# Performance work log

Measured on AMD Instinct MI355X. Metric: run time of the kernel, lower is better.

The kernel has to match this reference:

```python
import jax, jax.numpy as jnp
import numpy as np

N = 20000
E = 320000
IN_C = 256
HID = 64
OUT_C = 64
NUM_LAYERS = 3
HEADS = 8


def setup_inputs() -> dict:
    key = jax.random.key(0)
    ks = jax.random.split(key, 12)
    s_in = 1.0 / np.sqrt(IN_C)
    s_h = 1.0 / np.sqrt(HID)
    inp = {
        "x": jax.random.normal(ks[0], (N, IN_C), dtype=jnp.float32),
        "edge_index": jax.random.randint(ks[1], (2, E), 0, N, dtype=jnp.int64),
        "lin1_w": jax.random.uniform(ks[2], (IN_C, HID), jnp.float32, -s_in, s_in),
        "lin1_b": jnp.zeros((HID,), jnp.float32),
        "wq": jax.random.uniform(ks[3], (NUM_LAYERS, HID, HID), jnp.float32, -s_h, s_h),
        "bq": jnp.zeros((NUM_LAYERS, HID), jnp.float32),
        "wk": jax.random.uniform(ks[4], (NUM_LAYERS, HID, HID), jnp.float32, -s_h, s_h),
        "bk": jnp.zeros((NUM_LAYERS, HID), jnp.float32),
        "wv": jax.random.uniform(ks[5], (NUM_LAYERS, HID, HID), jnp.float32, -s_h, s_h),
        "bv": jnp.zeros((NUM_LAYERS, HID), jnp.float32),
        "lin2_w": jax.random.uniform(ks[6], (HID, OUT_C), jnp.float32, -s_h, s_h),
        "lin2_b": jnp.zeros((OUT_C,), jnp.float32),
    }
    return inp


def reference(x, edge_index, lin1_w, lin1_b, wq, bq, wk, bk, wv, bv, lin2_w, lin2_b):
    n = x.shape[0]
    C = lin1_w.shape[1]
    d = C // HEADS  # per-head dim
    inv_sqrt_d = 1.0 / (d ** 0.5)

    # gcn_norm with self-loops (symmetric normalization, edge weights = 1)
    loop = jnp.arange(n, dtype=edge_index.dtype)
    row = jnp.concatenate([edge_index[0], loop])  # source j
    col = jnp.concatenate([edge_index[1], loop])  # target i
    deg = jax.ops.segment_sum(jnp.ones_like(col, dtype=x.dtype), col, num_segments=n)
    dinv = jnp.where(deg > 0, deg ** -0.5, 0.0)
    norm = dinv[row] * dinv[col]  # [E+N]

    # input projection (dropout inactive in eval mode)
    h = jax.nn.relu(x @ lin1_w + lin1_b)
    x_all = h[:, None, :]  # [N, 1, C] growing history

    for l in range(NUM_LAYERS):
        t = x_all.shape[1]
        # node-level projections (linear commutes with gather)
        q = x_all[:, -1] @ wq[l] + bq[l]                      # [N, C]
        k = jnp.einsum("ntc,cd->ntd", x_all, wk[l]) + bk[l]   # [N, t, C]
        v = jnp.einsum("ntc,cd->ntd", x_all, wv[l]) + bv[l]   # [N, t, C]
        # per-edge multi-head attention of target's latest repr over source history
        Qe = q[col].reshape(-1, HEADS, d)                      # [E', H, d]
        Ke = k[row].reshape(-1, t, HEADS, d)                   # [E', t, H, d]
        Ve = v[row].reshape(-1, t, HEADS, d)
        scores = jnp.einsum("ehd,ethd->eht", Qe, Ke) * inv_sqrt_d
        attn = jax.nn.softmax(scores, axis=-1)                 # [E', H, t]
        msg = jnp.einsum("eht,ethd->ehd", attn, Ve).reshape(-1, C)
        msg = msg * norm[:, None]
        out = jax.ops.segment_sum(msg, col, num_segments=n)    # sum aggregation
        out = jax.nn.relu(out)
        x_all = jnp.concatenate([x_all, out[:, None, :]], axis=1)

    logits = x_all[:, -1] @ lin2_w + lin2_b
    return jax.nn.log_softmax(logits, axis=1)
```

## Files before the change

### kernel.cpp

```cpp
#include <hip/hip_runtime.h>
#include <math.h>

#define HID 64
#define HEADS 8
#define NUM_LAYERS 3

typedef __attribute__((ext_vector_type(8))) short bf16x8;
typedef __attribute__((ext_vector_type(4))) float f32x4;

__device__ __forceinline__ unsigned short f2bf(float f) {
    union { float f; unsigned int u; } cv; cv.f = f;
    unsigned int u = cv.u;
    unsigned int r = (u + 0x7FFFu + ((u >> 16) & 1u)) >> 16;
    return (unsigned short)r;
}
__device__ __forceinline__ float bflo(unsigned int u) {
    union { unsigned int u; float f; } cv; cv.u = u << 16; return cv.f;
}
__device__ __forceinline__ float bfhi(unsigned int u) {
    union { unsigned int u; float f; } cv; cv.u = u & 0xFFFF0000u; return cv.f;
}
__device__ __forceinline__ unsigned relu_pk(unsigned u) {
    unsigned m = ((u & 0x8000u) ? 0u : 0xFFFFu) |
                 ((u & 0x80000000u) ? 0u : 0xFFFF0000u);
    return u & m;
}

__global__ void k_count(const int* __restrict__ col, int* __restrict__ counts, int E) {
    int e = blockIdx.x * blockDim.x + threadIdx.x;
    if (e < E) atomicAdd(&counts[col[e]], 1);
}

__global__ __launch_bounds__(1024) void k_scan(const int* __restrict__ counts,
                                               int* __restrict__ start,
                                               float* __restrict__ dinv, int n) {
    __shared__ int wsum[16];
    int tid = threadIdx.x;
    int lane = tid & 63, wv = tid >> 6;
    int ipt = (n + 1023) >> 10;
    int c0 = tid * ipt;
    int c1 = min(n, c0 + ipt);
    int s = 0;
    for (int i = c0; i < c1; ++i) s += counts[i];
    int x = s;
#pragma unroll
    for (int off = 1; off < 64; off <<= 1) {
        int y = __shfl_up(x, off);
        if (lane >= off) x += y;
    }
    if (lane == 63) wsum[wv] = x;
    __syncthreads();
    if (wv == 0 && lane < 16) {
        int t2 = wsum[lane];
#pragma unroll
        for (int off = 1; off < 16; off <<= 1) {
            int y = __shfl_up(t2, off);
            if (lane >= off) t2 += y;
        }
        wsum[lane] = t2;
    }
    __syncthreads();
    int waveoff = (wv > 0) ? wsum[wv - 1] : 0;
    int run = waveoff + x - s;
    for (int i = c0; i < c1; ++i) {
        int v = counts[i];
        start[i] = run;
        dinv[i] = rsqrtf((float)(v + 1));
        run += v;
    }
    if (tid == 0) start[n] = wsum[15];
}

__global__ void k_scatter(const int* __restrict__ ei, const int* __restrict__ start,
                          int* __restrict__ fill, int* __restrict__ ebuf, int E) {
    int e = blockIdx.x * blockDim.x + threadIdx.x;
    if (e >= E) return;
    int r = ei[e], c = ei[E + e];
    int pos = start[c] + atomicAdd(&fill[c], 1);
    ebuf[pos] = r;
}

#define ALD 72

__device__ __forceinline__ void stage_w_bf16(unsigned short* Wt,
                                             const float* __restrict__ w, int tid) {
    for (int idx = tid; idx < 1024; idx += 256) {
        int k = idx >> 4, n4 = (idx & 15) * 4;
        float4 wv = *(const float4*)&w[k * 64 + n4];
        Wt[(n4 + 0) * ALD + k] = f2bf(wv.x);
        Wt[(n4 + 1) * ALD + k] = f2bf(wv.y);
        Wt[(n4 + 2) * ALD + k] = f2bf(wv.z);
        Wt[(n4 + 3) * ALD + k] = f2bf(wv.w);
    }
}

__device__ __forceinline__ void mfma_step(const unsigned short* Alds,
                                          const unsigned short* Wt,
                                          int tid, f32x4 acc[4]) {
    int lane = tid & 63;
    int m0 = (tid >> 6) * 16;
    int c16 = lane & 15, quad = lane >> 4;
    const unsigned short* ar = &Alds[(m0 + c16) * ALD + quad * 8];
    bf16x8 a0 = *(const bf16x8*)ar;
    bf16x8 a1 = *(const bf16x8*)(ar + 32);
#pragma unroll
    for (int nt = 0; nt < 4; ++nt) {
        const unsigned short* br = &Wt[(nt * 16 + c16) * ALD + quad * 8];
        bf16x8 b0 = *(const bf16x8*)br;
        bf16x8 b1 = *(const bf16x8*)(br + 32);
        acc[nt] = __builtin_amdgcn_mfma_f32_16x16x32_bf16(a0, b0, acc[nt], 0, 0, 0);
        acc[nt] = __builtin_amdgcn_mfma_f32_16x16x32_bf16(a1, b1, acc[nt], 0, 0, 0);
    }
}

__global__ __launch_bounds__(256, 4) void k_lin1(
    const float* __restrict__ x, const float* __restrict__ w,
    const float* __restrict__ b, const float* __restrict__ wv0,
    const float* __restrict__ bv0, unsigned short* __restrict__ h,
    unsigned short* __restrict__ kv, int n) {
    __shared__ __align__(16) unsigned short Alds[64 * ALD];
    __shared__ __align__(16) unsigned short Wt[64 * ALD];
    int tid = threadIdx.x;
    int node0 = blockIdx.x * 64;
    f32x4 acc[4];
#pragma unroll
    for (int nt = 0; nt < 4; ++nt) acc[nt] = (f32x4){0.f, 0.f, 0.f, 0.f};

    for (int kc = 0; kc < 256; kc += 64) {
        __syncthreads();
        stage_w_bf16(Wt, w + kc * 64, tid);
        for (int idx = tid; idx < 1024; idx += 256) {
            int r = idx >> 4, c4 = (idx & 15) * 4;
            int node = node0 + r;
            float4 v = make_float4(0.f, 0.f, 0.f, 0.f);
            if (node < n) v = *(const float4*)&x[(size_t)node * 256 + kc + c4];
            Alds[r * ALD + c4 + 0] = f2bf(v.x);
            Alds[r * ALD + c4 + 1] = f2bf(v.y);
            Alds[r * ALD + c4 + 2] = f2bf(v.z);
            Alds[r * ALD + c4 + 3] = f2bf(v.w);
        }
        __syncthreads();
        mfma_step(Alds, Wt, tid, acc);
    }
    int lane = tid & 63;
    int m0 = (tid >> 6) * 16, c16 = lane & 15, quad = lane >> 4;
    float bias[4];
#pragma unroll
    for (int nt = 0; nt < 4; ++nt) bias[nt] = b[nt * 16 + c16];

    __syncthreads();
    stage_w_bf16(Wt, wv0, tid);
#pragma unroll
    for (int i = 0; i < 4; ++i) {
        int row = m0 + quad * 4 + i;
        int node = node0 + row;
#pragma unroll
        for (int nt = 0; nt < 4; ++nt) {
            unsigned short hb = f2bf(fmaxf(acc[nt][i] + bias[nt], 0.f));
            Alds[row * ALD + nt * 16 + c16] = hb;
            if (node < n) h[(size_t)node * 64 + nt * 16 + c16] = hb;
        }
    }
    __syncthreads();
    f32x4 acc2[4];
#pragma unroll
    for (int nt = 0; nt < 4; ++nt) acc2[nt] = (f32x4){0.f, 0.f, 0.f, 0.f};
    mfma_step(Alds, Wt, tid, acc2);
    float bias2[4];
#pragma unroll
    for (int nt = 0; nt < 4; ++nt) bias2[nt] = bv0[nt * 16 + c16];
#pragma unroll
    for (int i = 0; i < 4; ++i) {
        int node = node0 + m0 + quad * 4 + i;
        if (node < n) {
#pragma unroll
            for (int nt = 0; nt < 4; ++nt)
                kv[(size_t)node * 64 + nt * 16 + c16] = f2bf(acc2[nt][i] + bias2[nt]);
        }
    }
}

__global__ __launch_bounds__(256, 4) void k_qkv(
    const unsigned short* __restrict__ xsbase,
    const float* __restrict__ wq, const float* __restrict__ bq,
    const float* __restrict__ wk, const float* __restrict__ bk,
    const float* __restrict__ wv, const float* __restrict__ bv,
    float* __restrict__ q, unsigned short* __restrict__ kv,
    int n, int layer, int t, int kv_stride) {
    int job = blockIdx.y;
    const unsigned short* src; const float* w; const float* b; bool relu_in;
    int kv_off = 0;
    if (job == 0) {
        src = xsbase + (size_t)layer * n * 64;
        w = wq + layer * 4096; b = bq + layer * 64;
        relu_in = (layer >= 1);
    } else if (job <= t) {
        int s = job - 1;
        src = xsbase + (size_t)s * n * 64;
        w = wk + layer * 4096; b = bk + layer * 64;
        kv_off = s * 128;
        relu_in = (s >= 1);
    } else {
        int s = job - t - 1;
        src = xsbase + (size_t)s * n * 64;
        w = wv + layer * 4096; b = bv + layer * 64;
        kv_off = s * 128 + 64;
        relu_in = (s >= 1);
    }
    __shared__ __align__(16) unsigned short Alds[64 * ALD];
    __shared__ __align__(16) unsigned short Wt[64 * ALD];
    int tid = threadIdx.x;
    int node0 = blockIdx.x * 64;
    stage_w_bf16(Wt, w, tid);
    for (int idx = tid; idx < 512; idx += 256) {
        int r = idx >> 3, seg = idx & 7;
        int node = node0 + r;
        uint4 u = make_uint4(0u, 0u, 0u, 0u);
        if (node < n) u = *(const uint4*)&src[(size_t)node * 64 + seg * 8];
        if (relu_in) {
            u.x = relu_pk(u.x); u.y = relu_pk(u.y);
            u.z = relu_pk(u.z); u.w = relu_pk(u.w);
        }
        *(uint4*)&Alds[r * ALD + seg * 8] = u;
    }
    __syncthreads();
    f32x4 acc[4];
#pragma unroll
    for (int nt = 0; nt < 4; ++nt) acc[nt] = (f32x4){0.f, 0.f, 0.f, 0.f};
    mfma_step(Alds, Wt, tid, acc);

    int lane = tid & 63;
    int m0 = (tid >> 6) * 16, c16 = lane & 15, quad = lane >> 4;
    float bias[4];
#pragma unroll
    for (int nt = 0; nt < 4; ++nt) bias[nt] = b[nt * 16 + c16];
    if (job == 0) {
#pragma unroll
        for (int i = 0; i < 4; ++i) {
            int node = node0 + m0 + quad * 4 + i;
            if (node < n) {
#pragma unroll
                for (int nt = 0; nt < 4; ++nt)
                    q[(size_t)node * 64 + nt * 16 + c16] = acc[nt][i] + bias[nt];
            }
        }
    } else {
#pragma unroll
        for (int i = 0; i < 4; ++i) {
            int node = node0 + m0 + quad * 4 + i;
            if (node < n) {
#pragma unroll
                for (int nt = 0; nt < 4; ++nt)
                    kv[(size_t)node * kv_stride + kv_off + nt * 16 + c16] =
                        f2bf(acc[nt][i] + bias[nt]);
            }
        }
    }
}

template <int T>
__global__ __launch_bounds__(256) void k_attn_g(
    const int* __restrict__ start, const int* __restrict__ ebuf,
    const float* __restrict__ dinv, const float* __restrict__ q,
    const unsigned short* __restrict__ kv, unsigned short* __restrict__ outp, int n) {
    const int KVS = (T == 1) ? 64 : T * 128;
    int node = (int)((blockIdx.x * (size_t)blockDim.x + threadIdx.x) >> 6);
    int lane = threadIdx.x & 63;
    if (node >= n) return;
    int g = lane >> 3;
    int cb = (lane & 7) * 8;
    const float isd = 0.35355339059327373f;

    float qv[8];
    if (T > 1) {
        float4 q0 = *(const float4*)&q[(size_t)node * 64 + cb];
        float4 q1 = *(const float4*)&q[(size_t)node * 64 + cb + 4];
        qv[0] = q0.x; qv[1] = q0.y; qv[2] = q0.z; qv[3] = q0.w;
        qv[4] = q1.x; qv[5] = q1.y; qv[6] = q1.z; qv[7] = q1.w;
    }
    float dc = dinv[node];
    int s0 = start[node];
    int cnt = start[node + 1] - s0 + 1;

    float acc[8];
#pragma unroll
    for (int k = 0; k < 8; ++k) acc[k] = 0.f;

    for (int base = 0; base < cnt; base += 8) {
        int idx = base + g;
        bool valid = idx < cnt;
        int r = node;
        if (valid && idx > 0) r = ebuf[s0 + idx - 1];
        float dr = valid ? dinv[r] : 0.f;
        const unsigned short* rkv = kv + (size_t)r * KVS;

        float sc[T];
        float wgt;
        if (T > 1) {
            float m = -1e30f;
#pragma unroll
            for (int s = 0; s < T; ++s) {
                uint4 ku = *(const uint4*)&rkv[s * 128 + cb];
                float p = qv[0] * bflo(ku.x) + qv[1] * bfhi(ku.x)
                        + qv[2] * bflo(ku.y) + qv[3] * bfhi(ku.y)
                        + qv[4] * bflo(ku.z) + qv[5] * bfhi(ku.z)
                        + qv[6] * bflo(ku.w) + qv[7] * bfhi(ku.w);
                p *= isd;
                sc[s] = p;
                m = fmaxf(m, p);
            }
            float denom = 0.f;
#pragma unroll
            for (int s = 0; s < T; ++s) { sc[s] = __expf(sc[s] - m); denom += sc[s]; }
            wgt = dr / denom;
        } else {
            sc[0] = 1.f;
            wgt = dr;
        }

        float mg[8];
#pragma unroll
        for (int k = 0; k < 8; ++k) mg[k] = 0.f;
#pragma unroll
        for (int s = 0; s < T; ++s) {
            uint4 vu = *(const uint4*)&rkv[((T == 1) ? 0 : s * 128 + 64) + cb];
            float wv_ = sc[s];
            mg[0] += wv_ * bflo(vu.x); mg[1] += wv_ * bfhi(vu.x);
            mg[2] += wv_ * bflo(vu.y); mg[3] += wv_ * bfhi(vu.y);
            mg[4] += wv_ * bflo(vu.z); mg[5] += wv_ * bfhi(vu.z);
            mg[6] += wv_ * bflo(vu.w); mg[7] += wv_ * bfhi(vu.w);
        }
#pragma unroll
        for (int k = 0; k < 8; ++k) acc[k] += wgt * mg[k];
    }

#pragma unroll
    for (int off = 8; off < 64; off <<= 1) {
#pragma unroll
        for (int k = 0; k < 8; ++k) acc[k] += __shfl_xor(acc[k], off);
    }
    if (g == 0) {
        ushort4 o0, o1;
        o0.x = f2bf(acc[0] * dc); o0.y = f2bf(acc[1] * dc);
        o0.z = f2bf(acc[2] * dc); o0.w = f2bf(acc[3] * dc);
        o1.x = f2bf(acc[4] * dc); o1.y = f2bf(acc[5] * dc);
        o1.z = f2bf(acc[6] * dc); o1.w = f2bf(acc[7] * dc);
        *(ushort4*)&outp[(size_t)node * 64 + cb] = o0;
        *(ushort4*)&outp[(size_t)node * 64 + cb + 4] = o1;
    }
}

__global__ __launch_bounds__(256) void k_attn3f(
    const int* __restrict__ start, const int* __restrict__ ebuf,
    const float* __restrict__ dinv, const float* __restrict__ q,
    const unsigned short* __restrict__ kv,
    const float* __restrict__ w2, const float* __restrict__ b2,
    float* __restrict__ outp, int n) {
    const int T = 3, KVS = 384;
    int node = (int)((blockIdx.x * (size_t)blockDim.x + threadIdx.x) >> 6);
    int lane = threadIdx.x & 63;
    if (node >= n) return;
    int g = lane >> 3;
    int cb = (lane & 7) * 8;
    const float isd = 0.35355339059327373f;

    float qv[8];
    {
        float4 q0 = *(const float4*)&q[(size_t)node * 64 + cb];
        float4 q1 = *(const float4*)&q[(size_t)node * 64 + cb + 4];
        qv[0] = q0.x; qv[1] = q0.y; qv[2] = q0.z; qv[3] = q0.w;
        qv[4] = q1.x; qv[5] = q1.y; qv[6] = q1.z; qv[7] = q1.w;
    }
    float dc = dinv[node];
    int s0 = start[node];
    int cnt = start[node + 1] - s0 + 1;

    float acc[8];
#pragma unroll
    for (int k = 0; k < 8; ++k) acc[k] = 0.f;

    for (int base = 0; base < cnt; base += 8) {
        int idx = base + g;
        bool valid = idx < cnt;
        int r = node;
        if (valid && idx > 0) r = ebuf[s0 + idx - 1];
        float dr = valid ? dinv[r] : 0.f;
        const unsigned short* rkv = kv + (size_t)r * KVS;

        float sc[T];
        float m = -1e30f;
#pragma unroll
        for (int s = 0; s < T; ++s) {
            uint4 ku = *(const uint4*)&rkv[s * 128 + cb];
            float p = qv[0] * bflo(ku.x) + qv[1] * bfhi(ku.x)
                    + qv[2] * bflo(ku.y) + qv[3] * bfhi(ku.y)
                    + qv[4] * bflo(ku.z) + qv[5] * bfhi(ku.z)
                    + qv[6] * bflo(ku.w) + qv[7] * bfhi(ku.w);
            p *= isd;
            sc[s] = p;
            m = fmaxf(m, p);
        }
        float denom = 0.f;
#pragma unroll
        for (int s = 0; s < T; ++s) { sc[s] = __expf(sc[s] - m); denom += sc[s]; }
        float wgt = dr / denom;

        float mg[8];
#pragma unroll
        for (int k = 0; k < 8; ++k) mg[k] = 0.f;
#pragma unroll
        for (int s = 0; s < T; ++s) {
            uint4 vu = *(const uint4*)&rkv[s * 128 + 64 + cb];
            float wv_ = sc[s];
            mg[0] += wv_ * bflo(vu.x); mg[1] += wv_ * bfhi(vu.x);
            mg[2] += wv_ * bflo(vu.y); mg[3] += wv_ * bfhi(vu.y);
            mg[4] += wv_ * bflo(vu.z); mg[5] += wv_ * bfhi(vu.z);
            mg[6] += wv_ * bflo(vu.w); mg[7] += wv_ * bfhi(vu.w);
        }
#pragma unroll
        for (int k = 0; k < 8; ++k) acc[k] += wgt * mg[k];
    }

#pragma unroll
    for (int off = 8; off < 64; off <<= 1) {
#pragma unroll
        for (int k = 0; k < 8; ++k) acc[k] += __shfl_xor(acc[k], off);
    }
    float lg = b2[lane];
#pragma unroll
    for (int c = 0; c < 64; ++c) {
        float xc = fmaxf(__shfl(acc[c & 7], c >> 3) * dc, 0.f);
        lg += xc * w2[c * 64 + lane];
    }
    float mx = lg;
#pragma unroll
    for (int off = 1; off < 64; off <<= 1) mx = fmaxf(mx, __shfl_xor(mx, off));
    float e = __expf(lg - mx);
    float ssum = e;
#pragma unroll
    for (int off = 1; off < 64; off <<= 1) ssum += __shfl_xor(ssum, off);
    outp[(size_t)node * 64 + lane] = lg - mx - __logf(ssum);
}

extern "C" void kernel_launch(void* const* d_in, const int* in_sizes, int n_in,
                              void* d_out, int out_size, void* d_ws, size_t ws_size,
                              hipStream_t stream) {
    const float* x  = (const float*)d_in[0];
    const int*   ei = (const int*)d_in[1];
    const float* w1 = (const float*)d_in[2];
    const float* b1 = (const float*)d_in[3];
    const float* wq = (const float*)d_in[4];
    const float* bq = (const float*)d_in[5];
    const float* wk = (const float*)d_in[6];
    const float* bk = (const float*)d_in[7];
    const float* wv = (const float*)d_in[8];
    const float* bv = (const float*)d_in[9];
    const float* w2 = (const float*)d_in[10];
    const float* b2 = (const float*)d_in[11];
    float* outp = (float*)d_out;

    int n = in_sizes[0] / 256;
    int E = in_sizes[1] / 2;

    float* ws = (float*)d_ws;
    size_t off = 0;
    float* dinv = ws + off; off += (size_t)n;
    float* q    = ws + off; off += (size_t)n * 64;
    unsigned short* xsU = (unsigned short*)(ws + off); off += (size_t)n * 96;
    unsigned short* kvU = (unsigned short*)(ws + off); off += (size_t)n * 192;
    int* wsI    = (int*)(ws + off);
    int* counts = wsI;
    int* fill   = wsI + n;
    int* startA = wsI + 2 * n;
    int* ebuf   = wsI + 3 * n + 1;

    hipMemsetAsync(counts, 0, 2 * (size_t)n * sizeof(int), stream);
    k_count<<<(E + 255) / 256, 256, 0, stream>>>(ei + E, counts, E);
    k_scan<<<1, 1024, 0, stream>>>(counts, startA, dinv, n);
    k_scatter<<<(E + 255) / 256, 256, 0, stream>>>(ei, startA, fill, ebuf, E);

    k_lin1<<<(n + 63) / 64, 256, 0, stream>>>(x, w1, b1, wv, bv, xsU, kvU, n);

    int attn_grid = (int)(((size_t)n * 64 + 255) / 256);

    k_attn_g<1><<<attn_grid, 256, 0, stream>>>(startA, ebuf, dinv, q, kvU,
                                               xsU + (size_t)n * 64, n);
    {
        dim3 grid((n + 63) / 64, 5);
        k_qkv<<<grid, 256, 0, stream>>>(xsU, wq, bq, wk, bk, wv, bv,
                                        q, kvU, n, 1, 2, 256);
        k_attn_g<2><<<attn_grid, 256, 0, stream>>>(startA, ebuf, dinv, q, kvU,
                                                   xsU + (size_t)n * 128, n);
    }
    {
        dim3 grid((n + 63) / 64, 7);
        k_qkv<<<grid, 256, 0, stream>>>(xsU, wq, bq, wk, bk, wv, bv,
                                        q, kvU, n, 2, 3, 384);
        k_attn3f<<<attn_grid, 256, 0, stream>>>(startA, ebuf, dinv, q, kvU,
                                                w2, b2, outp, n);
    }
}
```

Before: 265.6 us.

## Fold K/V projections into per-node query and aggregate raw history features

Removes the separate QKV projection kernels and K/V buffers. Each target node computes its own q, pre-multiplies it by Wk to get q', and scores each edge directly against the source's raw bf16 history (the bk term is dropped since it is constant across t and cancels in softmax). The attention-weighted history is aggregated, and Wv plus bias is applied once per node after summation. This trades per-node recompute and 64-step shuffle matvecs for much less gathered memory per edge. Edges are now processed serially per wave instead of 8 at a time, with shuffle reductions per edge, which lengthens the loop.

```diff
diff --git a/kernel.cpp b/kernel.cpp
--- a/kernel.cpp
+++ b/kernel.cpp
@@ -3,7 +3,7 @@
 
 #define HID 64
 #define HEADS 8
-#define NUM_LAYERS 3
+#define ALD 72
 
 typedef __attribute__((ext_vector_type(8))) short bf16x8;
 typedef __attribute__((ext_vector_type(4))) float f32x4;
@@ -20,10 +20,17 @@
 __device__ __forceinline__ float bfhi(unsigned int u) {
     union { unsigned int u; float f; } cv; cv.u = u & 0xFFFF0000u; return cv.f;
 }
-__device__ __forceinline__ unsigned relu_pk(unsigned u) {
-    unsigned m = ((u & 0x8000u) ? 0u : 0xFFFFu) |
-                 ((u & 0x80000000u) ? 0u : 0xFFFF0000u);
-    return u & m;
+
+__device__ __forceinline__ float dot8(const float* qp, uint4 u) {
+    return qp[0] * bflo(u.x) + qp[1] * bfhi(u.x) + qp[2] * bflo(u.y) +
+           qp[3] * bfhi(u.y) + qp[4] * bflo(u.z) + qp[5] * bfhi(u.z) +
+           qp[6] * bflo(u.w) + qp[7] * bfhi(u.w);
+}
+__device__ __forceinline__ void axpy8(float a, uint4 u, float* Y) {
+    Y[0] += a * bflo(u.x); Y[1] += a * bfhi(u.x);
+    Y[2] += a * bflo(u.y); Y[3] += a * bfhi(u.y);
+    Y[4] += a * bflo(u.z); Y[5] += a * bfhi(u.z);
+    Y[6] += a * bflo(u.w); Y[7] += a * bfhi(u.w);
 }
 
 __global__ void k_count(const int* __restrict__ col, int* __restrict__ counts, int E) {
@@ -36,7 +43,7 @@
                                                float* __restrict__ dinv, int n) {
     __shared__ int wsum[16];
     int tid = threadIdx.x;
-    int lane = tid & 63, wv = tid >> 6;
+    int lane = tid & 63, wvi = tid >> 6;
     int ipt = (n + 1023) >> 10;
     int c0 = tid * ipt;
     int c1 = min(n, c0 + ipt);
@@ -48,9 +55,9 @@
         int y = __shfl_up(x, off);
         if (lane >= off) x += y;
     }
-    if (lane == 63) wsum[wv] = x;
+    if (lane == 63) wsum[wvi] = x;
     __syncthreads();
-    if (wv == 0 && lane < 16) {
+    if (wvi == 0 && lane < 16) {
         int t2 = wsum[lane];
 #pragma unroll
         for (int off = 1; off < 16; off <<= 1) {
@@ -60,7 +67,7 @@
         wsum[lane] = t2;
     }
     __syncthreads();
-    int waveoff = (wv > 0) ? wsum[wv - 1] : 0;
+    int waveoff = (wvi > 0) ? wsum[wvi - 1] : 0;
     int run = waveoff + x - s;
     for (int i = c0; i < c1; ++i) {
         int v = counts[i];
@@ -79,8 +86,6 @@
     int pos = start[c] + atomicAdd(&fill[c], 1);
     ebuf[pos] = r;
 }
-
-#define ALD 72
 
 __device__ __forceinline__ void stage_w_bf16(unsigned short* Wt,
                                              const float* __restrict__ w, int tid) {
@@ -115,9 +120,7 @@
 
 __global__ __launch_bounds__(256, 4) void k_lin1(
     const float* __restrict__ x, const float* __restrict__ w,
-    const float* __restrict__ b, const float* __restrict__ wv0,
-    const float* __restrict__ bv0, unsigned short* __restrict__ h,
-    unsigned short* __restrict__ kv, int n) {
+    const float* __restrict__ b, unsigned short* __restrict__ h, int n) {
     __shared__ __align__(16) unsigned short Alds[64 * ALD];
     __shared__ __align__(16) unsigned short Wt[64 * ALD];
     int tid = threadIdx.x;
@@ -147,299 +150,134 @@
     float bias[4];
 #pragma unroll
     for (int nt = 0; nt < 4; ++nt) bias[nt] = b[nt * 16 + c16];
-
-    __syncthreads();
-    stage_w_bf16(Wt, wv0, tid);
-#pragma unroll
-    for (int i = 0; i < 4; ++i) {
-        int row = m0 + quad * 4 + i;
-        int node = node0 + row;
-#pragma unroll
-        for (int nt = 0; nt < 4; ++nt) {
-            unsigned short hb = f2bf(fmaxf(acc[nt][i] + bias[nt], 0.f));
-            Alds[row * ALD + nt * 16 + c16] = hb;
-            if (node < n) h[(size_t)node * 64 + nt * 16 + c16] = hb;
-        }
-    }
-    __syncthreads();
-    f32x4 acc2[4];
-#pragma unroll
-    for (int nt = 0; nt < 4; ++nt) acc2[nt] = (f32x4){0.f, 0.f, 0.f, 0.f};
-    mfma_step(Alds, Wt, tid, acc2);
-    float bias2[4];
-#pragma unroll
-    for (int nt = 0; nt < 4; ++nt) bias2[nt] = bv0[nt * 16 + c16];
 #pragma unroll
     for (int i = 0; i < 4; ++i) {
         int node = node0 + m0 + quad * 4 + i;
         if (node < n) {
 #pragma unroll
             for (int nt = 0; nt < 4; ++nt)
-                kv[(size_t)node * 64 + nt * 16 + c16] = f2bf(acc2[nt][i] + bias2[nt]);
-        }
-    }
-}
-
-__global__ __launch_bounds__(256, 4) void k_qkv(
-    const unsigned short* __restrict__ xsbase,
+                h[(size_t)node * 64 + nt * 16 + c16] =
+                    f2bf(fmaxf(acc[nt][i] + bias[nt], 0.f));
+        }
+    }
+}
+
+template <int T, bool FINAL>
+__device__ __forceinline__ void attn_x_body(
+    int node, int lane, const int* __restrict__ start,
+    const int* __restrict__ ebuf, const float* __restrict__ dinv,
+    unsigned short* __restrict__ xs, size_t sstride,
     const float* __restrict__ wq, const float* __restrict__ bq,
-    const float* __restrict__ wk, const float* __restrict__ bk,
-    const float* __restrict__ wv, const float* __restrict__ bv,
-    float* __restrict__ q, unsigned short* __restrict__ kv,
-    int n, int layer, int t, int kv_stride) {
-    int job = blockIdx.y;
-    const unsigned short* src; const float* w; const float* b; bool relu_in;
-    int kv_off = 0;
-    if (job == 0) {
-        src = xsbase + (size_t)layer * n * 64;
-        w = wq + layer * 4096; b = bq + layer * 64;
-        relu_in = (layer >= 1);
-    } else if (job <= t) {
-        int s = job - 1;
-        src = xsbase + (size_t)s * n * 64;
-        w = wk + layer * 4096; b = bk + layer * 64;
-        kv_off = s * 128;
-        relu_in = (s >= 1);
-    } else {
-        int s = job - t - 1;
-        src = xsbase + (size_t)s * n * 64;
-        w = wv + layer * 4096; b = bv + layer * 64;
-        kv_off = s * 128 + 64;
-        relu_in = (s >= 1);
-    }
-    __shared__ __align__(16) unsigned short Alds[64 * ALD];
-    __shared__ __align__(16) unsigned short Wt[64 * ALD];
-    int tid = threadIdx.x;
-    int node0 = blockIdx.x * 64;
-    stage_w_bf16(Wt, w, tid);
-    for (int idx = tid; idx < 512; idx += 256) {
-        int r = idx >> 3, seg = idx & 7;
-        int node = node0 + r;
-        uint4 u = make_uint4(0u, 0u, 0u, 0u);
-        if (node < n) u = *(const uint4*)&src[(size_t)node * 64 + seg * 8];
-        if (relu_in) {
-            u.x = relu_pk(u.x); u.y = relu_pk(u.y);
-            u.z = relu_pk(u.z); u.w = relu_pk(u.w);
-        }
-        *(uint4*)&Alds[r * ALD + seg * 8] = u;
-    }
-    __syncthreads();
-    f32x4 acc[4];
-#pragma unroll
-    for (int nt = 0; nt < 4; ++nt) acc[nt] = (f32x4){0.f, 0.f, 0.f, 0.f};
-    mfma_step(Alds, Wt, tid, acc);
-
-    int lane = tid & 63;
-    int m0 = (tid >> 6) * 16, c16 = lane & 15, quad = lane >> 4;
-    float bias[4];
-#pragma unroll
-    for (int nt = 0; nt < 4; ++nt) bias[nt] = b[nt * 16 + c16];
-    if (job == 0) {
-#pragma unroll
-        for (int i = 0; i < 4; ++i) {
-            int node = node0 + m0 + quad * 4 + i;
-            if (node < n) {
-#pragma unroll
-                for (int nt = 0; nt < 4; ++nt)
-                    q[(size_t)node * 64 + nt * 16 + c16] = acc[nt][i] + bias[nt];
-            }
-        }
-    } else {
-#pragma unroll
-        for (int i = 0; i < 4; ++i) {
-            int node = node0 + m0 + quad * 4 + i;
-            if (node < n) {
-#pragma unroll
-                for (int nt = 0; nt < 4; ++nt)
-                    kv[(size_t)node * kv_stride + kv_off + nt * 16 + c16] =
-                        f2bf(acc[nt][i] + bias[nt]);
-            }
-        }
-    }
-}
-
-template <int T>
-__global__ __launch_bounds__(256) void k_attn_g(
-    const int* __restrict__ start, const int* __restrict__ ebuf,
-    const float* __restrict__ dinv, const float* __restrict__ q,
-    const unsigned short* __restrict__ kv, unsigned short* __restrict__ outp, int n) {
-    const int KVS = (T == 1) ? 64 : T * 128;
-    int node = (int)((blockIdx.x * (size_t)blockDim.x + threadIdx.x) >> 6);
-    int lane = threadIdx.x & 63;
-    if (node >= n) return;
-    int g = lane >> 3;
-    int cb = (lane & 7) * 8;
-    const float isd = 0.35355339059327373f;
-
-    float qv[8];
+    const float* __restrict__ wk, const float* __restrict__ wv,
+    const float* __restrict__ bv, const float* __restrict__ w2,
+    const float* __restrict__ b2, float* __restrict__ outf) {
+    const int h8 = lane & 56;
+    const int cb = (lane & 7) * 8;
+
+    float qp[8];
     if (T > 1) {
-        float4 q0 = *(const float4*)&q[(size_t)node * 64 + cb];
-        float4 q1 = *(const float4*)&q[(size_t)node * 64 + cb + 4];
-        qv[0] = q0.x; qv[1] = q0.y; qv[2] = q0.z; qv[3] = q0.w;
-        qv[4] = q1.x; qv[5] = q1.y; qv[6] = q1.z; qv[7] = q1.w;
-    }
+        const float isd = 0.35355339059327373f;
+        uint4 xu = *(const uint4*)&xs[(size_t)(T - 1) * sstride +
+                                      (size_t)node * 64 + cb];
+        float xq[8] = {bflo(xu.x), bfhi(xu.x), bflo(xu.y), bfhi(xu.y),
+                       bflo(xu.z), bfhi(xu.z), bflo(xu.w), bfhi(xu.w)};
+        float qo = bq[lane];
+#pragma unroll
+        for (int c = 0; c < 64; ++c)
+            qo += __shfl(xq[c & 7], c >> 3) * wq[c * 64 + lane];
+        float qh[8];
+#pragma unroll
+        for (int d = 0; d < 8; ++d) qh[d] = __shfl(qo, h8 + d);
+#pragma unroll
+        for (int dp = 0; dp < 8; ++dp) {
+            const float* wr = &wk[(cb + dp) * 64 + h8];
+            float s = 0.f;
+#pragma unroll
+            for (int d = 0; d < 8; ++d) s += qh[d] * wr[d];
+            qp[dp] = s * isd;
+        }
+    }
+
     float dc = dinv[node];
     int s0 = start[node];
     int cnt = start[node + 1] - s0 + 1;
 
-    float acc[8];
-#pragma unroll
-    for (int k = 0; k < 8; ++k) acc[k] = 0.f;
-
-    for (int base = 0; base < cnt; base += 8) {
-        int idx = base + g;
-        bool valid = idx < cnt;
+    float Y[8];
+#pragma unroll
+    for (int d = 0; d < 8; ++d) Y[d] = 0.f;
+    float S = 0.f;
+
+    for (int idx = 0; idx < cnt; ++idx) {
         int r = node;
-        if (valid && idx > 0) r = ebuf[s0 + idx - 1];
-        float dr = valid ? dinv[r] : 0.f;
-        const unsigned short* rkv = kv + (size_t)r * KVS;
-
-        float sc[T];
-        float wgt;
+        if (idx > 0) r = ebuf[s0 + idx - 1];
+        float dr = dinv[r];
+        uint4 xu[T];
+#pragma unroll
+        for (int t = 0; t < T; ++t)
+            xu[t] = *(const uint4*)&xs[(size_t)t * sstride + (size_t)r * 64 + cb];
+        float coef[T];
         if (T > 1) {
-            float m = -1e30f;
-#pragma unroll
-            for (int s = 0; s < T; ++s) {
-                uint4 ku = *(const uint4*)&rkv[s * 128 + cb];
-                float p = qv[0] * bflo(ku.x) + qv[1] * bfhi(ku.x)
-                        + qv[2] * bflo(ku.y) + qv[3] * bfhi(ku.y)
-                        + qv[4] * bflo(ku.z) + qv[5] * bfhi(ku.z)
-                        + qv[6] * bflo(ku.w) + qv[7] * bfhi(ku.w);
-                p *= isd;
-                sc[s] = p;
-                m = fmaxf(m, p);
+            float p[T];
+#pragma unroll
+            for (int t = 0; t < T; ++t) p[t] = dot8(qp, xu[t]);
+#pragma unroll
+            for (int off = 1; off < 8; off <<= 1) {
+#pragma unroll
+                for (int t = 0; t < T; ++t) p[t] += __shfl_xor(p[t], off);
             }
+            float m = p[0];
+#pragma unroll
+            for (int t = 1; t < T; ++t) m = fmaxf(m, p[t]);
             float denom = 0.f;
 #pragma unroll
-            for (int s = 0; s < T; ++s) { sc[s] = __expf(sc[s] - m); denom += sc[s]; }
-            wgt = dr / denom;
+            for (int t = 0; t < T; ++t) { coef[t] = __expf(p[t] - m); denom += coef[t]; }
+            float w = dr / denom;
+#pragma unroll
+            for (int t = 0; t < T; ++t) coef[t] *= w;
         } else {
-            sc[0] = 1.f;
-            wgt = dr;
-        }
-
-        float mg[8];
-#pragma unroll
-        for (int k = 0; k < 8; ++k) mg[k] = 0.f;
-#pragma unroll
-        for (int s = 0; s < T; ++s) {
-            uint4 vu = *(const uint4*)&rkv[((T == 1) ? 0 : s * 128 + 64) + cb];
-            float wv_ = sc[s];
-            mg[0] += wv_ * bflo(vu.x); mg[1] += wv_ * bfhi(vu.x);
-            mg[2] += wv_ * bflo(vu.y); mg[3] += wv_ * bfhi(vu.y);
-            mg[4] += wv_ * bflo(vu.z); mg[5] += wv_ * bfhi(vu.z);
-            mg[6] += wv_ * bflo(vu.w); mg[7] += wv_ * bfhi(vu.w);
-        }
-#pragma unroll
-        for (int k = 0; k < 8; ++k) acc[k] += wgt * mg[k];
-    }
-
-#pragma unroll
-    for (int off = 8; off < 64; off <<= 1) {
-#pragma unroll
-        for (int k = 0; k < 8; ++k) acc[k] += __shfl_xor(acc[k], off);
-    }
-    if (g == 0) {
-        ushort4 o0, o1;
-        o0.x = f2bf(acc[0] * dc); o0.y = f2bf(acc[1] * dc);
-        o0.z = f2bf(acc[2] * dc); o0.w = f2bf(acc[3] * dc);
-        o1.x = f2bf(acc[4] * dc); o1.y = f2bf(acc[5] * dc);
-        o1.z = f2bf(acc[6] * dc); o1.w = f2bf(acc[7] * dc);
-        *(ushort4*)&outp[(size_t)node * 64 + cb] = o0;
-        *(ushort4*)&outp[(size_t)node * 64 + cb + 4] = o1;
-    }
-}
-
-__global__ __launch_bounds__(256) void k_attn3f(
+            coef[0] = dr;
+        }
+#pragma unroll
+        for (int t = 0; t < T; ++t) axpy8(coef[t], xu[t], Y);
+        S += dr;
+    }
+
+    float v = bv[lane] * S;
+#pragma unroll
+    for (int c = 0; c < 64; ++c)
+        v += __shfl(Y[c & 7], h8 | (c >> 3)) * wv[c * 64 + lane];
+    float out = fmaxf(v * dc, 0.f);
+
+    if (!FINAL) {
+        xs[(size_t)T * sstride + (size_t)node * 64 + lane] = f2bf(out);
+    } else {
+        float lg = b2[lane];
+#pragma unroll
+        for (int c = 0; c < 64; ++c)
+            lg += __shfl(out, c) * w2[c * 64 + lane];
+        float mx = lg;
+#pragma unroll
+        for (int off = 1; off < 64; off <<= 1) mx = fmaxf(mx, __shfl_xor(mx, off));
+        float e = __expf(lg - mx);
+        float ssum = e;
+#pragma unroll
+        for (int off = 1; off < 64; off <<= 1) ssum += __shfl_xor(ssum, off);
+        outf[(size_t)node * 64 + lane] = lg - mx - __logf(ssum);
+    }
+}
+
+template <int T, bool FINAL>
+__global__ __launch_bounds__(256, 4) void k_attn_x(
     const int* __restrict__ start, const int* __restrict__ ebuf,
-    const float* __restrict__ dinv, const float* __restrict__ q,
-    const unsigned short* __restrict__ kv,
-    const float* __restrict__ w2, const float* __restrict__ b2,
-    float* __restrict__ outp, int n) {
-    const int T = 3, KVS = 384;
+    const float* __restrict__ dinv, unsigned short* __restrict__ xs,
+    size_t sstride, const float* __restrict__ wq, const float* __restrict__ bq,
+    const float* __restrict__ wk, const float* __restrict__ wv,
+    const float* __restrict__ bv, const float* __restrict__ w2,
+    const float* __restrict__ b2, float* __restrict__ outf, int n) {
     int node = (int)((blockIdx.x * (size_t)blockDim.x + threadIdx.x) >> 6);
-    int lane = threadIdx.x & 63;
     if (node >= n) return;
-    int g = lane >> 3;
-    int cb = (lane & 7) * 8;
-    const float isd = 0.35355339059327373f;
-
-    float qv[8];
-    {
-        float4 q0 = *(const float4*)&q[(size_t)node * 64 + cb];
-        float4 q1 = *(const float4*)&q[(size_t)node * 64 + cb + 4];
-        qv[0] = q0.x; qv[1] = q0.y; qv[2] = q0.z; qv[3] = q0.w;
-        qv[4] = q1.x; qv[5] = q1.y; qv[6] = q1.z; qv[7] = q1.w;
-    }
-    float dc = dinv[node];
-    int s0 = start[node];
-    int cnt = start[node + 1] - s0 + 1;
-
-    float acc[8];
-#pragma unroll
-    for (int k = 0; k < 8; ++k) acc[k] = 0.f;
-
-    for (int base = 0; base < cnt; base += 8) {
-        int idx = base + g;
-        bool valid = idx < cnt;
-        int r = node;
-        if (valid && idx > 0) r = ebuf[s0 + idx - 1];
-        float dr = valid ? dinv[r] : 0.f;
-        const unsigned short* rkv = kv + (size_t)r * KVS;
-
-        float sc[T];
-        float m = -1e30f;
-#pragma unroll
-        for (int s = 0; s < T; ++s) {
-            uint4 ku = *(const uint4*)&rkv[s * 128 + cb];
-            float p = qv[0] * bflo(ku.x) + qv[1] * bfhi(ku.x)
-                    + qv[2] * bflo(ku.y) + qv[3] * bfhi(ku.y)
-                    + qv[4] * bflo(ku.z) + qv[5] * bfhi(ku.z)
-                    + qv[6] * bflo(ku.w) + qv[7] * bfhi(ku.w);
-            p *= isd;
-            sc[s] = p;
-            m = fmaxf(m, p);
-        }
-        float denom = 0.f;
-#pragma unroll
-        for (int s = 0; s < T; ++s) { sc[s] = __expf(sc[s] - m); denom += sc[s]; }
-        float wgt = dr / denom;
-
-        float mg[8];
-#pragma unroll
-        for (int k = 0; k < 8; ++k) mg[k] = 0.f;
-#pragma unroll
-        for (int s = 0; s < T; ++s) {
-            uint4 vu = *(const uint4*)&rkv[s * 128 + 64 + cb];
-            float wv_ = sc[s];
-            mg[0] += wv_ * bflo(vu.x); mg[1] += wv_ * bfhi(vu.x);
-            mg[2] += wv_ * bflo(vu.y); mg[3] += wv_ * bfhi(vu.y);
-            mg[4] += wv_ * bflo(vu.z); mg[5] += wv_ * bfhi(vu.z);
-            mg[6] += wv_ * bflo(vu.w); mg[7] += wv_ * bfhi(vu.w);
-        }
-#pragma unroll
-        for (int k = 0; k < 8; ++k) acc[k] += wgt * mg[k];
-    }
-
-#pragma unroll
-    for (int off = 8; off < 64; off <<= 1) {
-#pragma unroll
-        for (int k = 0; k < 8; ++k) acc[k] += __shfl_xor(acc[k], off);
-    }
-    float lg = b2[lane];
-#pragma unroll
-    for (int c = 0; c < 64; ++c) {
-        float xc = fmaxf(__shfl(acc[c & 7], c >> 3) * dc, 0.f);
-        lg += xc * w2[c * 64 + lane];
-    }
-    float mx = lg;
-#pragma unroll
-    for (int off = 1; off < 64; off <<= 1) mx = fmaxf(mx, __shfl_xor(mx, off));
-    float e = __expf(lg - mx);
-    float ssum = e;
-#pragma unroll
-    for (int off = 1; off < 64; off <<= 1) ssum += __shfl_xor(ssum, off);
-    outp[(size_t)node * 64 + lane] = lg - mx - __logf(ssum);
+    attn_x_body<T, FINAL>(node, threadIdx.x & 63, start, ebuf, dinv, xs, sstride,
+                          wq, bq, wk, wv, bv, w2, b2, outf);
 }
 
 extern "C" void kernel_launch(void* const* d_in, const int* in_sizes, int n_in,
@@ -458,6 +296,7 @@
     const float* w2 = (const float*)d_in[10];
     const float* b2 = (const float*)d_in[11];
     float* outp = (float*)d_out;
+    (void)bk;
 
     int n = in_sizes[0] / 256;
     int E = in_sizes[1] / 2;
@@ -465,38 +304,33 @@
     float* ws = (float*)d_ws;
     size_t off = 0;
     float* dinv = ws + off; off += (size_t)n;
-    float* q    = ws + off; off += (size_t)n * 64;
     unsigned short* xsU = (unsigned short*)(ws + off); off += (size_t)n * 96;
-    unsigned short* kvU = (unsigned short*)(ws + off); off += (size_t)n * 192;
     int* wsI    = (int*)(ws + off);
     int* counts = wsI;
     int* fill   = wsI + n;
     int* startA = wsI + 2 * n;
     int* ebuf   = wsI + 3 * n + 1;
 
+    size_t sstride = (size_t)n * 64;
+
     hipMemsetAsync(counts, 0, 2 * (size_t)n * sizeof(int), stream);
     k_count<<<(E + 255) / 256, 256, 0, stream>>>(ei + E, counts, E);
     k_scan<<<1, 1024, 0, stream>>>(counts, startA, dinv, n);
     k_scatter<<<(E + 255) / 256, 256, 0, stream>>>(ei, startA, fill, ebuf, E);
 
-    k_lin1<<<(n + 63) / 64, 256, 0, stream>>>(x, w1, b1, wv, bv, xsU, kvU, n);
+    k_lin1<<<(n + 63) / 64, 256, 0, stream>>>(x, w1, b1, xsU, n);
 
     int attn_grid = (int)(((size_t)n * 64 + 255) / 256);
 
-    k_attn_g<1><<<attn_grid, 256, 0, stream>>>(startA, ebuf, dinv, q, kvU,
-                                               xsU + (size_t)n * 64, n);
-    {
-        dim3 grid((n + 63) / 64, 5);
-        k_qkv<<<grid, 256, 0, stream>>>(xsU, wq, bq, wk, bk, wv, bv,
-                                        q, kvU, n, 1, 2, 256);
-        k_attn_g<2><<<attn_grid, 256, 0, stream>>>(startA, ebuf, dinv, q, kvU,
-                                                   xsU + (size_t)n * 128, n);
-    }
-    {
-        dim3 grid((n + 63) / 64, 7);
-        k_qkv<<<grid, 256, 0, stream>>>(xsU, wq, bq, wk, bk, wv, bv,
-                                        q, kvU, n, 2, 3, 384);
-        k_attn3f<<<attn_grid, 256, 0, stream>>>(startA, ebuf, dinv, q, kvU,
-                                                w2, b2, outp, n);
-    }
-}
+    k_attn_x<1, false><<<attn_grid, 256, 0, stream>>>(
+        startA, ebuf, dinv, xsU, sstride, nullptr, nullptr, nullptr,
+        wv, bv, nullptr, nullptr, nullptr, n);
+
+    k_attn_x<2, false><<<attn_grid, 256, 0, stream>>>(
+        startA, ebuf, dinv, xsU, sstride, wq + 4096, bq + 64, wk + 4096,
+        wv + 4096, bv + 64, nullptr, nullptr, nullptr, n);
+
+    k_attn_x<3, true><<<attn_grid, 256, 0, stream>>>(
+        startA, ebuf, dinv, xsU, sstride, wq + 8192, bq + 128, wk + 8192,
+        wv + 8192, bv + 128, w2, b2, outp, n);
+}
```

Measured after the change: 499.7 us. 1.88x slower.

## Fuse Q projection into attention, batch K/V staging, compact edge buffer

Applied to the files above, without the earlier changes.

The Q projection now runs inside the attention kernel as a per-node wave GEMV, which removes the fp32 q buffer and its round trip. The K/V projections for layers 1 and 2 that depend only on earlier states are computed together in one staged launch, so the per-layer launch only handles the newest state. The edge-source buffer is stored as 16-bit indices, the fill counter is replaced by decrementing counts, and the neighbor index load is prefetched one chunk ahead. The trade-offs are redundant Q matmul work per wave, more shuffles, and a 16-bit index that only holds for n ≤ 65536.

```diff
diff --git a/kernel.cpp b/kernel.cpp
--- a/kernel.cpp
+++ b/kernel.cpp
@@ -3,7 +3,7 @@
 
 #define HID 64
 #define HEADS 8
-#define NUM_LAYERS 3
+#define ALD 72
 
 typedef __attribute__((ext_vector_type(8))) short bf16x8;
 typedef __attribute__((ext_vector_type(4))) float f32x4;
@@ -36,7 +36,7 @@
                                                float* __restrict__ dinv, int n) {
     __shared__ int wsum[16];
     int tid = threadIdx.x;
-    int lane = tid & 63, wv = tid >> 6;
+    int lane = tid & 63, wvi = tid >> 6;
     int ipt = (n + 1023) >> 10;
     int c0 = tid * ipt;
     int c1 = min(n, c0 + ipt);
@@ -48,9 +48,9 @@
         int y = __shfl_up(x, off);
         if (lane >= off) x += y;
     }
-    if (lane == 63) wsum[wv] = x;
+    if (lane == 63) wsum[wvi] = x;
     __syncthreads();
-    if (wv == 0 && lane < 16) {
+    if (wvi == 0 && lane < 16) {
         int t2 = wsum[lane];
 #pragma unroll
         for (int off = 1; off < 16; off <<= 1) {
@@ -60,7 +60,7 @@
         wsum[lane] = t2;
     }
     __syncthreads();
-    int waveoff = (wv > 0) ? wsum[wv - 1] : 0;
+    int waveoff = (wvi > 0) ? wsum[wvi - 1] : 0;
     int run = waveoff + x - s;
     for (int i = c0; i < c1; ++i) {
         int v = counts[i];
@@ -72,15 +72,14 @@
 }
 
 __global__ void k_scatter(const int* __restrict__ ei, const int* __restrict__ start,
-                          int* __restrict__ fill, int* __restrict__ ebuf, int E) {
+                          int* __restrict__ counts, unsigned short* __restrict__ ebuf,
+                          int E) {
     int e = blockIdx.x * blockDim.x + threadIdx.x;
     if (e >= E) return;
     int r = ei[e], c = ei[E + e];
-    int pos = start[c] + atomicAdd(&fill[c], 1);
-    ebuf[pos] = r;
-}
-
-#define ALD 72
+    int pos = start[c] + atomicSub(&counts[c], 1) - 1;
+    ebuf[pos] = (unsigned short)r;
+}
 
 __device__ __forceinline__ void stage_w_bf16(unsigned short* Wt,
                                              const float* __restrict__ w, int tid) {
@@ -180,33 +179,24 @@
     }
 }
 
-__global__ __launch_bounds__(256, 4) void k_qkv(
-    const unsigned short* __restrict__ xsbase,
-    const float* __restrict__ wq, const float* __restrict__ bq,
+__global__ __launch_bounds__(256, 4) void k_stage(
+    const unsigned short* __restrict__ xs, size_t sstride,
     const float* __restrict__ wk, const float* __restrict__ bk,
     const float* __restrict__ wv, const float* __restrict__ bv,
-    float* __restrict__ q, unsigned short* __restrict__ kv,
-    int n, int layer, int t, int kv_stride) {
-    int job = blockIdx.y;
-    const unsigned short* src; const float* w; const float* b; bool relu_in;
-    int kv_off = 0;
-    if (job == 0) {
-        src = xsbase + (size_t)layer * n * 64;
-        w = wq + layer * 4096; b = bq + layer * 64;
-        relu_in = (layer >= 1);
-    } else if (job <= t) {
-        int s = job - 1;
-        src = xsbase + (size_t)s * n * 64;
-        w = wk + layer * 4096; b = bk + layer * 64;
-        kv_off = s * 128;
-        relu_in = (s >= 1);
-    } else {
-        int s = job - t - 1;
-        src = xsbase + (size_t)s * n * 64;
-        w = wv + layer * 4096; b = bv + layer * 64;
-        kv_off = s * 128 + 64;
-        relu_in = (s >= 1);
-    }
+    unsigned short* __restrict__ kv1, unsigned short* __restrict__ kv2,
+    int n, int phase) {
+    int j = blockIdx.y;
+    int layer, s, isV;
+    if (phase == 0) { layer = 1 + (j >> 2); s = j & 1; isV = (j >> 1) & 1; }
+    else            { layer = 2; s = 2; isV = j; }
+    const unsigned short* src = xs + (size_t)s * sstride;
+    const float* w = (isV ? wv : wk) + layer * 4096;
+    const float* b = (isV ? bv : bk) + layer * 64;
+    unsigned short* dst = (layer == 1) ? kv1 : kv2;
+    int stride = (layer == 1) ? 256 : 384;
+    int koff = s * 128 + (isV ? 64 : 0);
+    bool relu_in = (s >= 1);
+
     __shared__ __align__(16) unsigned short Alds[64 * ALD];
     __shared__ __align__(16) unsigned short Wt[64 * ALD];
     int tid = threadIdx.x;
@@ -234,50 +224,50 @@
     float bias[4];
 #pragma unroll
     for (int nt = 0; nt < 4; ++nt) bias[nt] = b[nt * 16 + c16];
-    if (job == 0) {
-#pragma unroll
-        for (int i = 0; i < 4; ++i) {
-            int node = node0 + m0 + quad * 4 + i;
-            if (node < n) {
-#pragma unroll
-                for (int nt = 0; nt < 4; ++nt)
-                    q[(size_t)node * 64 + nt * 16 + c16] = acc[nt][i] + bias[nt];
-            }
-        }
-    } else {
-#pragma unroll
-        for (int i = 0; i < 4; ++i) {
-            int node = node0 + m0 + quad * 4 + i;
-            if (node < n) {
-#pragma unroll
-                for (int nt = 0; nt < 4; ++nt)
-                    kv[(size_t)node * kv_stride + kv_off + nt * 16 + c16] =
-                        f2bf(acc[nt][i] + bias[nt]);
-            }
-        }
-    }
-}
-
-template <int T>
-__global__ __launch_bounds__(256) void k_attn_g(
-    const int* __restrict__ start, const int* __restrict__ ebuf,
-    const float* __restrict__ dinv, const float* __restrict__ q,
-    const unsigned short* __restrict__ kv, unsigned short* __restrict__ outp, int n) {
+#pragma unroll
+    for (int i = 0; i < 4; ++i) {
+        int node = node0 + m0 + quad * 4 + i;
+        if (node < n) {
+#pragma unroll
+            for (int nt = 0; nt < 4; ++nt)
+                dst[(size_t)node * stride + koff + nt * 16 + c16] =
+                    f2bf(acc[nt][i] + bias[nt]);
+        }
+    }
+}
+
+template <int T, bool FINAL>
+__global__ __launch_bounds__(256) void k_attn(
+    const int* __restrict__ start, const unsigned short* __restrict__ ebuf,
+    const float* __restrict__ dinv, const unsigned short* __restrict__ xs,
+    size_t sstride, const unsigned short* __restrict__ kv,
+    const float* __restrict__ wq, const float* __restrict__ bq,
+    const float* __restrict__ w2, const float* __restrict__ b2,
+    unsigned short* __restrict__ outb, float* __restrict__ outf, int n) {
     const int KVS = (T == 1) ? 64 : T * 128;
     int node = (int)((blockIdx.x * (size_t)blockDim.x + threadIdx.x) >> 6);
     int lane = threadIdx.x & 63;
     if (node >= n) return;
     int g = lane >> 3;
     int cb = (lane & 7) * 8;
-    const float isd = 0.35355339059327373f;
 
     float qv[8];
     if (T > 1) {
-        float4 q0 = *(const float4*)&q[(size_t)node * 64 + cb];
-        float4 q1 = *(const float4*)&q[(size_t)node * 64 + cb + 4];
-        qv[0] = q0.x; qv[1] = q0.y; qv[2] = q0.z; qv[3] = q0.w;
-        qv[4] = q1.x; qv[5] = q1.y; qv[6] = q1.z; qv[7] = q1.w;
-    }
+        const float isd = 0.35355339059327373f;
+        uint4 xu = *(const uint4*)&xs[(size_t)(T - 1) * sstride +
+                                      (size_t)node * 64 + cb];
+        float xq[8] = {fmaxf(bflo(xu.x), 0.f), fmaxf(bfhi(xu.x), 0.f),
+                       fmaxf(bflo(xu.y), 0.f), fmaxf(bfhi(xu.y), 0.f),
+                       fmaxf(bflo(xu.z), 0.f), fmaxf(bfhi(xu.z), 0.f),
+                       fmaxf(bflo(xu.w), 0.f), fmaxf(bfhi(xu.w), 0.f)};
+        float qo = bq[lane];
+#pragma unroll
+        for (int c = 0; c < 64; ++c)
+            qo += __shfl(xq[c & 7], c >> 3) * wq[c * 64 + lane];
+#pragma unroll
+        for (int d = 0; d < 8; ++d) qv[d] = __shfl(qo, (lane & 7) * 8 + d) * isd;
+    }
+
     float dc = dinv[node];
     int s0 = start[node];
     int cnt = start[node + 1] - s0 + 1;
@@ -286,13 +276,20 @@
 #pragma unroll
     for (int k = 0; k < 8; ++k) acc[k] = 0.f;
 
-    for (int base = 0; base < cnt; base += 8) {
-        int idx = base + g;
-        bool valid = idx < cnt;
-        int r = node;
-        if (valid && idx > 0) r = ebuf[s0 + idx - 1];
-        float dr = valid ? dinv[r] : 0.f;
-        const unsigned short* rkv = kv + (size_t)r * KVS;
+    int nch = (cnt + 7) >> 3;
+    int idx = g;
+    bool v_cur = idx < cnt;
+    int r_cur = node;
+    if (v_cur && idx > 0) r_cur = ebuf[s0 + idx - 1];
+
+    for (int c = 0; c < nch; ++c) {
+        int idxn = idx + 8;
+        bool v_nxt = idxn < cnt;
+        int r_nxt = node;
+        if (v_nxt) r_nxt = ebuf[s0 + idxn - 1];
+
+        float dr = v_cur ? dinv[r_cur] : 0.f;
+        const unsigned short* rkv = kv + (size_t)r_cur * KVS;
 
         float sc[T];
         float wgt;
@@ -305,7 +302,6 @@
                         + qv[2] * bflo(ku.y) + qv[3] * bfhi(ku.y)
                         + qv[4] * bflo(ku.z) + qv[5] * bfhi(ku.z)
                         + qv[6] * bflo(ku.w) + qv[7] * bfhi(ku.w);
-                p *= isd;
                 sc[s] = p;
                 m = fmaxf(m, p);
             }
@@ -332,6 +328,8 @@
         }
 #pragma unroll
         for (int k = 0; k < 8; ++k) acc[k] += wgt * mg[k];
+
+        r_cur = r_nxt; v_cur = v_nxt; idx = idxn;
     }
 
 #pragma unroll
@@ -339,107 +337,33 @@
 #pragma unroll
         for (int k = 0; k < 8; ++k) acc[k] += __shfl_xor(acc[k], off);
     }
-    if (g == 0) {
-        ushort4 o0, o1;
-        o0.x = f2bf(acc[0] * dc); o0.y = f2bf(acc[1] * dc);
-        o0.z = f2bf(acc[2] * dc); o0.w = f2bf(acc[3] * dc);
-        o1.x = f2bf(acc[4] * dc); o1.y = f2bf(acc[5] * dc);
-        o1.z = f2bf(acc[6] * dc); o1.w = f2bf(acc[7] * dc);
-        *(ushort4*)&outp[(size_t)node * 64 + cb] = o0;
-        *(ushort4*)&outp[(size_t)node * 64 + cb + 4] = o1;
-    }
-}
-
-__global__ __launch_bounds__(256) void k_attn3f(
-    const int* __restrict__ start, const int* __restrict__ ebuf,
-    const float* __restrict__ dinv, const float* __restrict__ q,
-    const unsigned short* __restrict__ kv,
-    const float* __restrict__ w2, const float* __restrict__ b2,
-    float* __restrict__ outp, int n) {
-    const int T = 3, KVS = 384;
-    int node = (int)((blockIdx.x * (size_t)blockDim.x + threadIdx.x) >> 6);
-    int lane = threadIdx.x & 63;
-    if (node >= n) return;
-    int g = lane >> 3;
-    int cb = (lane & 7) * 8;
-    const float isd = 0.35355339059327373f;
-
-    float qv[8];
-    {
-        float4 q0 = *(const float4*)&q[(size_t)node * 64 + cb];
-        float4 q1 = *(const float4*)&q[(size_t)node * 64 + cb + 4];
-        qv[0] = q0.x; qv[1] = q0.y; qv[2] = q0.z; qv[3] = q0.w;
-        qv[4] = q1.x; qv[5] = q1.y; qv[6] = q1.z; qv[7] = q1.w;
-    }
-    float dc = dinv[node];
-    int s0 = start[node];
-    int cnt = start[node + 1] - s0 + 1;
-
-    float acc[8];
-#pragma unroll
-    for (int k = 0; k < 8; ++k) acc[k] = 0.f;
-
-    for (int base = 0; base < cnt; base += 8) {
-        int idx = base + g;
-        bool valid = idx < cnt;
-        int r = node;
-        if (valid && idx > 0) r = ebuf[s0 + idx - 1];
-        float dr = valid ? dinv[r] : 0.f;
-        const unsigned short* rkv = kv + (size_t)r * KVS;
-
-        float sc[T];
-        float m = -1e30f;
-#pragma unroll
-        for (int s = 0; s < T; ++s) {
-            uint4 ku = *(const uint4*)&rkv[s * 128 + cb];
-            float p = qv[0] * bflo(ku.x) + qv[1] * bfhi(ku.x)
-                    + qv[2] * bflo(ku.y) + qv[3] * bfhi(ku.y)
-                    + qv[4] * bflo(ku.z) + qv[5] * bfhi(ku.z)
-                    + qv[6] * bflo(ku.w) + qv[7] * bfhi(ku.w);
-            p *= isd;
-            sc[s] = p;
-            m = fmaxf(m, p);
-        }
-        float denom = 0.f;
-#pragma unroll
-        for (int s = 0; s < T; ++s) { sc[s] = __expf(sc[s] - m); denom += sc[s]; }
-        float wgt = dr / denom;
-
-        float mg[8];
-#pragma unroll
-        for (int k = 0; k < 8; ++k) mg[k] = 0.f;
-#pragma unroll
-        for (int s = 0; s < T; ++s) {
-            uint4 vu = *(const uint4*)&rkv[s * 128 + 64 + cb];
-            float wv_ = sc[s];
-            mg[0] += wv_ * bflo(vu.x); mg[1] += wv_ * bfhi(vu.x);
-            mg[2] += wv_ * bflo(vu.y); mg[3] += wv_ * bfhi(vu.y);
-            mg[4] += wv_ * bflo(vu.z); mg[5] += wv_ * bfhi(vu.z);
-            mg[6] += wv_ * bflo(vu.w); mg[7] += wv_ * bfhi(vu.w);
-        }
-#pragma unroll
-        for (int k = 0; k < 8; ++k) acc[k] += wgt * mg[k];
-    }
-
-#pragma unroll
-    for (int off = 8; off < 64; off <<= 1) {
-#pragma unroll
-        for (int k = 0; k < 8; ++k) acc[k] += __shfl_xor(acc[k], off);
-    }
-    float lg = b2[lane];
-#pragma unroll
-    for (int c = 0; c < 64; ++c) {
-        float xc = fmaxf(__shfl(acc[c & 7], c >> 3) * dc, 0.f);
-        lg += xc * w2[c * 64 + lane];
-    }
-    float mx = lg;
-#pragma unroll
-    for (int off = 1; off < 64; off <<= 1) mx = fmaxf(mx, __shfl_xor(mx, off));
-    float e = __expf(lg - mx);
-    float ssum = e;
-#pragma unroll
-    for (int off = 1; off < 64; off <<= 1) ssum += __shfl_xor(ssum, off);
-    outp[(size_t)node * 64 + lane] = lg - mx - __logf(ssum);
+
+    if (!FINAL) {
+        if (g == 0) {
+            ushort4 o0, o1;
+            o0.x = f2bf(acc[0] * dc); o0.y = f2bf(acc[1] * dc);
+            o0.z = f2bf(acc[2] * dc); o0.w = f2bf(acc[3] * dc);
+            o1.x = f2bf(acc[4] * dc); o1.y = f2bf(acc[5] * dc);
+            o1.z = f2bf(acc[6] * dc); o1.w = f2bf(acc[7] * dc);
+            *(ushort4*)&outb[(size_t)node * 64 + cb] = o0;
+            *(ushort4*)&outb[(size_t)node * 64 + cb + 4] = o1;
+        }
+    } else {
+        float lg = b2[lane];
+#pragma unroll
+        for (int c = 0; c < 64; ++c) {
+            float xc = fmaxf(__shfl(acc[c & 7], c >> 3) * dc, 0.f);
+            lg += xc * w2[c * 64 + lane];
+        }
+        float mx = lg;
+#pragma unroll
+        for (int off = 1; off < 64; off <<= 1) mx = fmaxf(mx, __shfl_xor(mx, off));
+        float e = __expf(lg - mx);
+        float ssum = e;
+#pragma unroll
+        for (int off = 1; off < 64; off <<= 1) ssum += __shfl_xor(ssum, off);
+        outf[(size_t)node * 64 + lane] = lg - mx - __logf(ssum);
+    }
 }
 
 extern "C" void kernel_launch(void* const* d_in, const int* in_sizes, int n_in,
@@ -465,38 +389,46 @@
     float* ws = (float*)d_ws;
     size_t off = 0;
     float* dinv = ws + off; off += (size_t)n;
-    float* q    = ws + off; off += (size_t)n * 64;
     unsigned short* xsU = (unsigned short*)(ws + off); off += (size_t)n * 96;
-    unsigned short* kvU = (unsigned short*)(ws + off); off += (size_t)n * 192;
+    unsigned short* kv0 = (unsigned short*)(ws + off); off += (size_t)n * 32;
+    unsigned short* kv1 = (unsigned short*)(ws + off); off += (size_t)n * 128;
+    unsigned short* kv2 = (unsigned short*)(ws + off); off += (size_t)n * 192;
     int* wsI    = (int*)(ws + off);
     int* counts = wsI;
-    int* fill   = wsI + n;
-    int* startA = wsI + 2 * n;
-    int* ebuf   = wsI + 3 * n + 1;
-
-    hipMemsetAsync(counts, 0, 2 * (size_t)n * sizeof(int), stream);
+    int* startA = wsI + n;
+    unsigned short* ebuf = (unsigned short*)(wsI + 2 * n + 1);
+
+    size_t sstride = (size_t)n * 64;
+
+    hipMemsetAsync(counts, 0, (size_t)n * sizeof(int), stream);
     k_count<<<(E + 255) / 256, 256, 0, stream>>>(ei + E, counts, E);
     k_scan<<<1, 1024, 0, stream>>>(counts, startA, dinv, n);
-    k_scatter<<<(E + 255) / 256, 256, 0, stream>>>(ei, startA, fill, ebuf, E);
-
-    k_lin1<<<(n + 63) / 64, 256, 0, stream>>>(x, w1, b1, wv, bv, xsU, kvU, n);
+    k_scatter<<<(E + 255) / 256, 256, 0, stream>>>(ei, startA, counts, ebuf, E);
+
+    k_lin1<<<(n + 63) / 64, 256, 0, stream>>>(x, w1, b1, wv, bv, xsU, kv0, n);
 
     int attn_grid = (int)(((size_t)n * 64 + 255) / 256);
-
-    k_attn_g<1><<<attn_grid, 256, 0, stream>>>(startA, ebuf, dinv, q, kvU,
-                                               xsU + (size_t)n * 64, n);
+    int NT = (n + 63) / 64;
+
+    k_attn<1, false><<<attn_grid, 256, 0, stream>>>(
+        startA, ebuf, dinv, xsU, sstride, kv0, nullptr, nullptr, nullptr, nullptr,
+        xsU + sstride, nullptr, n);
+
     {
-        dim3 grid((n + 63) / 64, 5);
-        k_qkv<<<grid, 256, 0, stream>>>(xsU, wq, bq, wk, bk, wv, bv,
-                                        q, kvU, n, 1, 2, 256);
-        k_attn_g<2><<<attn_grid, 256, 0, stream>>>(startA, ebuf, dinv, q, kvU,
-                                                   xsU + (size_t)n * 128, n);
-    }
+        dim3 grid(NT, 8);
+        k_stage<<<grid, 256, 0, stream>>>(xsU, sstride, wk, bk, wv, bv,
+                                          kv1, kv2, n, 0);
+    }
+    k_attn<2, false><<<attn_grid, 256, 0, stream>>>(
+        startA, ebuf, dinv, xsU, sstride, kv1, wq + 4096, bq + 64, nullptr, nullptr,
+        xsU + 2 * sstride, nullptr, n);
+
     {
-        dim3 grid((n + 63) / 64, 7);
-        k_qkv<<<grid, 256, 0, stream>>>(xsU, wq, bq, wk, bk, wv, bv,
-                                        q, kvU, n, 2, 3, 384);
-        k_attn3f<<<attn_grid, 256, 0, stream>>>(startA, ebuf, dinv, q, kvU,
-                                                w2, b2, outp, n);
-    }
-}
+        dim3 grid(NT, 2);
+        k_stage<<<grid, 256, 0, stream>>>(xsU, sstride, wk, bk, wv, bv,
+                                          kv1, kv2, n, 1);
+    }
+    k_attn<3, true><<<attn_grid, 256, 0, stream>>>(
+        startA, ebuf, dinv, xsU, sstride, kv2, wq + 8192, bq + 128, w2, b2,
+        nullptr, outp, n);
+}
```

Measured after the change: 285.7 us. +7.6%, slower.
